# Optimization experiments

Hardware: AMD Instinct MI355X
Metric: run time of the kernel (lower is better)

The kernel has to match this reference:

```python
import jax, jax.numpy as jnp
import numpy as np

B, L, H_IN = 2, 512, 768
E = 256          # hidden_size
N = 12           # num_labels


def setup_inputs() -> dict:
    key = jax.random.key(0)
    ks = jax.random.split(key, 10)
    lim_in = 1.0 / np.sqrt(H_IN)
    lim_e = 1.0 / np.sqrt(E)
    lim_2e = 1.0 / np.sqrt(2 * E)
    return {
        "x":    jax.random.normal(ks[0], (B, L, H_IN), dtype=jnp.float32),
        "sW":   jax.random.uniform(ks[1], (E, H_IN), jnp.float32, -lim_in, lim_in),
        "sb":   jax.random.uniform(ks[2], (E,), jnp.float32, -lim_in, lim_in),
        "tW":   jax.random.uniform(ks[3], (E, H_IN), jnp.float32, -lim_in, lim_in),
        "tb":   jax.random.uniform(ks[4], (E,), jnp.float32, -lim_in, lim_in),
        "f2W":  jax.random.uniform(ks[5], (E, 2 * E), jnp.float32, -lim_2e, lim_2e),
        "f2b":  jax.random.uniform(ks[6], (E,), jnp.float32, -lim_2e, lim_2e),
        "f3W":  jax.random.normal(ks[7], (N, E), dtype=jnp.float32),  # init_weights: normal_
        "f3b":  jax.random.uniform(ks[8], (N,), jnp.float32, -lim_e, lim_e),
        "blW":  jax.random.normal(ks[9], (E * N, E), dtype=jnp.float32),  # bi_linear, no bias
    }


def reference(x, sW, sb, tW, tb, f2W, f2b, f3W, f3b, blW):
    b, l, _ = x.shape
    s = jax.nn.relu(x @ sW.T + sb)  # [B,L,E]
    t = jax.nn.relu(x @ tW.T + tb)  # [B,L,E]
    # biaffine term: key[b,s,e,n] = (s @ blW.T) reshaped, then key @ t^T
    key = (s @ blW.T).reshape(b, l, E, N)             # [B,L,E,N]
    out1 = jnp.einsum('bsen,ble->bsnl', key, t)       # [B,S,N,L]
    # pairwise concat-MLP, decomposed: cat(u,v) @ f2W.T == u@Wu.T + v@Wv.T
    Wu, Wv = f2W[:, :E], f2W[:, E:]
    su = s @ Wu.T                                     # [B,L,E]
    tv = t @ Wv.T                                     # [B,L,E]
    h = jax.nn.relu(su[:, :, None, :] + tv[:, None, :, :] + f2b)  # [B,L,L,E]
    out2 = h @ f3W.T + f3b                            # [B,L,L,N]
    out2 = jnp.transpose(out2, (0, 1, 3, 2))          # [B,L,N,L]
    return out1 + out2
```

## Files before the change

kernel.cpp:

```cpp
#include <hip/hip_runtime.h>
#include <hip/hip_bf16.h>


typedef unsigned short u16;
typedef __attribute__((ext_vector_type(8))) short    s16x8;
typedef __attribute__((ext_vector_type(8))) _Float16 f16x8;
typedef __attribute__((ext_vector_type(4))) float    f32x4;

__device__ inline u16 f2h(float f) { return __builtin_bit_cast(u16, (_Float16)f); }

__device__ inline void barrier_lds() {
    __builtin_amdgcn_sched_barrier(0);
    asm volatile("s_waitcnt lgkmcnt(0)" ::: "memory");
    __builtin_amdgcn_s_barrier();
    __builtin_amdgcn_sched_barrier(0);
}

__device__ inline s16x8 cvt2(float4 a, float4 b) {
    f16x8 h;
    h[0] = (_Float16)a.x; h[1] = (_Float16)a.y; h[2] = (_Float16)a.z; h[3] = (_Float16)a.w;
    h[4] = (_Float16)b.x; h[5] = (_Float16)b.y; h[6] = (_Float16)b.z; h[7] = (_Float16)b.w;
    return __builtin_bit_cast(s16x8, h);
}

__device__ inline f16x8 relu8(f16x8 v) {
#if __has_builtin(__builtin_elementwise_max)
    f16x8 z = {};
    return __builtin_elementwise_max(v, z);
#else
#pragma unroll
    for (int q = 0; q < 8; ++q) v[q] = v[q] > (_Float16)0.f ? v[q] : (_Float16)0.f;
    return v;
#endif
}

__device__ inline f32x4 mfma_f16(s16x8 a, s16x8 b, f32x4 c) {
    return __builtin_amdgcn_mfma_f32_16x16x32_f16(
        __builtin_bit_cast(f16x8, a), __builtin_bit_cast(f16x8, b), c, 0, 0, 0);
}
__device__ inline f32x4 mfma_f16v(f16x8 a, s16x8 b, f32x4 c) {
    return __builtin_amdgcn_mfma_f32_16x16x32_f16(a, __builtin_bit_cast(f16x8, b), c, 0, 0, 0);
}

__global__ __launch_bounds__(256, 3)
void prep_kernel(const float* __restrict__ x, const float* __restrict__ sW,
                 const float* __restrict__ tW, const float* __restrict__ sb,
                 const float* __restrict__ tb, const float* __restrict__ f2W,
                 const float* __restrict__ blW, const float* __restrict__ f3W,
                 u16* __restrict__ STb, u16* __restrict__ blkw, u16* __restrict__ f3wb)
{
    if (blockIdx.x >= 256) {
        int idx = (blockIdx.x - 256) * 256 + threadIdx.x;
        float4 v;
        u16* dst;
        if (idx < 229376) {
            int i4 = idx * 4;
            int r = i4 >> 8, k = i4 & 255;
            const float* src;
            if (r < 3072)      { int n = r >> 8, e = r & 255; src = &blW[(e * 12 + n) * 256 + k]; }
            else if (r < 3328) { src = &f2W[(r - 3072) * 512 + k]; }
            else               { src = &f2W[(r - 3328) * 512 + 256 + k]; }
            v = *(const float4*)src;
            dst = &blkw[i4];
        } else {
            int i4 = (idx - 229376) * 4;
            int row = i4 >> 8, e = i4 & 255;
            if (row < 12) v = *(const float4*)&f3W[row * 256 + e];
            else          v = make_float4(0.f, 0.f, 0.f, 0.f);
            dst = &f3wb[i4];
        }
        ushort4 o;
        o.x = f2h(v.x); o.y = f2h(v.y); o.z = f2h(v.z); o.w = f2h(v.w);
        *(ushort4*)dst = o;
        return;
    }
    __shared__ u16 As[64 * 72];
    __shared__ u16 Bs[32 * 72];
    const int tid = threadIdx.x;
    const int g = blockIdx.x;
    const int xcd = g & 7, slot = g >> 3;
    const int m0 = (((xcd << 1) | (slot >> 4))) * 64;
    const int n0 = (slot & 15) * 32;
    const int w = tid >> 6, l = tid & 63;
    const int wr = (w >> 1) * 32, wc = (w & 1) * 16;
    const int lr = l & 15, lg = l >> 4;
    const int srow = tid >> 2, kq = tid & 3;

    const float* ap = &x[(size_t)(m0 + srow) * 768 + kq * 16];
    const bool bstg = (tid < 128);
    const float* bp = nullptr;
    if (bstg) {
        int br = n0 + (tid >> 2);
        bp = (br < 256) ? &sW[(size_t)br * 768 + kq * 16]
                        : &tW[(size_t)(br - 256) * 768 + kq * 16];
    }
    float4 ra0 = *(const float4*)(ap + 0),  ra1 = *(const float4*)(ap + 4);
    float4 ra2 = *(const float4*)(ap + 8),  ra3 = *(const float4*)(ap + 12);
    float4 rb0, rb1, rb2, rb3;
    if (bstg) {
        rb0 = *(const float4*)(bp + 0);  rb1 = *(const float4*)(bp + 4);
        rb2 = *(const float4*)(bp + 8);  rb3 = *(const float4*)(bp + 12);
    }

    f32x4 acc[2] = {};
    for (int k0 = 0; k0 < 768; k0 += 64) {
        barrier_lds();
        *(s16x8*)&As[srow * 72 + kq * 16]     = cvt2(ra0, ra1);
        *(s16x8*)&As[srow * 72 + kq * 16 + 8] = cvt2(ra2, ra3);
        if (bstg) {
            *(s16x8*)&Bs[(tid >> 2) * 72 + kq * 16]     = cvt2(rb0, rb1);
            *(s16x8*)&Bs[(tid >> 2) * 72 + kq * 16 + 8] = cvt2(rb2, rb3);
        }
        barrier_lds();
        if (k0 + 64 < 768) {
            ra0 = *(const float4*)(ap + k0 + 64 + 0);  ra1 = *(const float4*)(ap + k0 + 64 + 4);
            ra2 = *(const float4*)(ap + k0 + 64 + 8);  ra3 = *(const float4*)(ap + k0 + 64 + 12);
            if (bstg) {
                rb0 = *(const float4*)(bp + k0 + 64 + 0);  rb1 = *(const float4*)(bp + k0 + 64 + 4);
                rb2 = *(const float4*)(bp + k0 + 64 + 8);  rb3 = *(const float4*)(bp + k0 + 64 + 12);
            }
        }
#pragma unroll
        for (int kk = 0; kk < 64; kk += 32) {
            s16x8 af[2], bf;
            af[0] = *(const s16x8*)&As[(wr      + lr) * 72 + kk + lg * 8];
            af[1] = *(const s16x8*)&As[(wr + 16 + lr) * 72 + kk + lg * 8];
            bf    = *(const s16x8*)&Bs[(wc      + lr) * 72 + kk + lg * 8];
            acc[0] = mfma_f16(af[0], bf, acc[0]);
            acc[1] = mfma_f16(af[1], bf, acc[1]);
        }
    }
#pragma unroll
    for (int fi = 0; fi < 2; ++fi) {
#pragma unroll
        for (int r = 0; r < 4; ++r) {
            int grow = m0 + wr + fi * 16 + lg * 4 + r;
            int gcol = n0 + wc + lr;
            float bias = (gcol < 256) ? sb[gcol] : tb[gcol - 256];
            float v = fmaxf(acc[fi][r] + bias, 0.f);
            STb[(size_t)grow * 512 + gcol] = f2h(v);
        }
    }
}

__global__ __launch_bounds__(256, 6)
void gemm_kst(const u16* __restrict__ STb, const u16* __restrict__ BLKW,
              const float* __restrict__ f2b,
              u16* __restrict__ KEYF, u16* __restrict__ SUp, u16* __restrict__ TVp)
{
    __shared__ u16 As[64 * 72];
    __shared__ u16 Bs[64 * 72];
    const int tid = threadIdx.x;
    const int lin = blockIdx.x + blockIdx.y * 56;
    const int xcd = lin & 7, slot = lin >> 3;
    const int n0 = (xcd * 7 + (slot >> 4)) * 64;
    const int m0 = (slot & 15) * 64;
    const int w = tid >> 6, l = tid & 63;
    const int wr = (w >> 1) * 32, wc = (w & 1) * 32;
    const int lr = l & 15, lg = l >> 4;
    const int srow = tid >> 2, kq = tid & 3;

    const u16* A = STb + (n0 >= 3328 ? 256 : 0);
    const u16* ap = &A[(size_t)(m0 + srow) * 512];
    const u16* bp = &BLKW[(size_t)(n0 + srow) * 256];
    s16x8 ra0 = *(const s16x8*)&ap[kq * 8];
    s16x8 ra1 = *(const s16x8*)&ap[(kq + 4) * 8];
    s16x8 rb0 = *(const s16x8*)&bp[kq * 8];
    s16x8 rb1 = *(const s16x8*)&bp[(kq + 4) * 8];

    f32x4 acc[2][2] = {};
    for (int k0 = 0; k0 < 256; k0 += 64) {
        barrier_lds();
        *(s16x8*)&As[srow * 72 + kq * 8]       = ra0;
        *(s16x8*)&As[srow * 72 + (kq + 4) * 8] = ra1;
        *(s16x8*)&Bs[srow * 72 + kq * 8]       = rb0;
        *(s16x8*)&Bs[srow * 72 + (kq + 4) * 8] = rb1;
        barrier_lds();
        if (k0 + 64 < 256) {
            ra0 = *(const s16x8*)&ap[k0 + 64 + kq * 8];
            ra1 = *(const s16x8*)&ap[k0 + 64 + (kq + 4) * 8];
            rb0 = *(const s16x8*)&bp[k0 + 64 + kq * 8];
            rb1 = *(const s16x8*)&bp[k0 + 64 + (kq + 4) * 8];
        }
#pragma unroll
        for (int kk = 0; kk < 64; kk += 32) {
            s16x8 af[2], bf[2];
            af[0] = *(const s16x8*)&As[(wr      + lr) * 72 + kk + lg * 8];
            af[1] = *(const s16x8*)&As[(wr + 16 + lr) * 72 + kk + lg * 8];
            bf[0] = *(const s16x8*)&Bs[(wc      + lr) * 72 + kk + lg * 8];
            bf[1] = *(const s16x8*)&Bs[(wc + 16 + lr) * 72 + kk + lg * 8];
#pragma unroll
            for (int fi = 0; fi < 2; ++fi)
#pragma unroll
                for (int fj = 0; fj < 2; ++fj)
                    acc[fi][fj] = mfma_f16(af[fi], bf[fj], acc[fi][fj]);
        }
    }
#pragma unroll
    for (int fi = 0; fi < 2; ++fi) {
#pragma unroll
        for (int fj = 0; fj < 2; ++fj) {
#pragma unroll
            for (int r = 0; r < 4; ++r) {
                int grow = m0 + wr + fi * 16 + lg * 4 + r;
                int gcol = n0 + wc + fj * 16 + lr;
                float v = acc[fi][fj][r];
                if (gcol < 3072) {
                    int n = gcol >> 8, e = gcol & 255;
                    int g2 = grow >> 4, li = grow & 15;
                    int it = e >> 5, sub = (e >> 3) & 3, eo = e & 7;
                    KEYF[((((size_t)n * 64 + g2) * 8 + it) * 64 + sub * 16 + li) * 8 + eo] = f2h(v);
                } else if (gcol < 3328) {
                    SUp[(size_t)grow * 256 + (gcol - 3072)] = f2h(v);
                } else {
                    TVp[(size_t)grow * 256 + (gcol - 3328)] = f2h(v + f2b[gcol - 3328]);
                }
            }
        }
    }
}

__global__ __launch_bounds__(512, 4)
void fused_out(const u16* __restrict__ KEYF, const u16* __restrict__ STb,
               const u16* __restrict__ SUp, const u16* __restrict__ TVp,
               const u16* __restrict__ F3WH, const float* __restrict__ f3b,
               float* __restrict__ out)
{
    __shared__ __align__(16) char smem[26624];
    u16* lds = (u16*)smem;
    const int TC0 = 0, SUC0 = 5120, F3C = 6400;

    const int tid = threadIdx.x;
    const int w = tid >> 6, l = tid & 63;

    const int lin  = blockIdx.x + (blockIdx.y << 3) + (blockIdx.z << 8);
    const int orig = (lin & 7) * 64 + (lin >> 3);
    const int j0 = (orig & 7) * 64;
    const int i0 = ((orig >> 3) & 31) * 16;
    const int b  = orig >> 8;

    const int lr = l & 15, lg = l >> 4;
    const int wn = w & 3, jh = w >> 2;

    const u16* src1 = nullptr; int d1 = 0, dstride = 0;
    if (tid < 256) {
        int jj = tid >> 2, qq = tid & 3;
        src1 = STb + (size_t)(b * 512 + j0 + jj) * 512 + 256 + qq * 8;
        d1 = TC0 + jj * 40 + qq * 8;
        dstride = 2560;
    } else if (tid < 320) {
        int q = tid - 256, ii = q >> 2, qq = q & 3;
        src1 = SUp + (size_t)(b * 512 + i0 + ii) * 256 + qq * 8;
        d1 = SUC0 + ii * 40 + qq * 8;
        dstride = 640;
    }
    const bool stg = (tid < 320);

    {
        int row = tid >> 5, qq = tid & 31;
        *(s16x8*)&lds[F3C + row * 264 + qq * 8] = *(const s16x8*)&F3WH[row * 256 + qq * 8];
    }

    const int gblk = b * 32 + (i0 >> 4);
    const u16* kfb0 = KEYF + ((size_t)((3 * wn + 0) * 64 + gblk) * 8) * 512 + l * 8;
    const u16* kfb1 = KEYF + ((size_t)((3 * wn + 1) * 64 + gblk) * 8) * 512 + l * 8;
    const u16* kfb2 = KEYF + ((size_t)((3 * wn + 2) * 64 + gblk) * 8) * 512 + l * 8;
    const u16* tvb = TVp + (size_t)(b * 512 + j0 + w * 8) * 256 + lg * 8;

    s16x8 r1 = {};
    if (stg) {
        r1 = *(const s16x8*)src1;
        *(s16x8*)&lds[d1] = r1;
        r1 = *(const s16x8*)(src1 + 32);
    }
    s16x8 kf0 = *(const s16x8*)kfb0;
    s16x8 kf1 = *(const s16x8*)kfb1;
    s16x8 kf2 = *(const s16x8*)kfb2;
    barrier_lds();

    f32x4 acc1[3][2] = {};
    f32x4 acc2[8]    = {};

#pragma unroll
    for (int it = 0; it < 8; ++it) {
        const int cur = it & 1, nxt = cur ^ 1;
        if (it < 7 && stg) *(s16x8*)&lds[d1 + nxt * dstride] = r1;
        s16x8 tf0 = *(const s16x8*)&lds[TC0 + cur * 2560 + (jh * 32      + lr) * 40 + lg * 8];
        s16x8 tf1 = *(const s16x8*)&lds[TC0 + cur * 2560 + (jh * 32 + 16 + lr) * 40 + lg * 8];
        acc1[0][0] = mfma_f16(kf0, tf0, acc1[0][0]);
        acc1[0][1] = mfma_f16(kf0, tf1, acc1[0][1]);
        acc1[1][0] = mfma_f16(kf1, tf0, acc1[1][0]);
        acc1[1][1] = mfma_f16(kf1, tf1, acc1[1][1]);
        acc1[2][0] = mfma_f16(kf2, tf0, acc1[2][0]);
        acc1[2][1] = mfma_f16(kf2, tf1, acc1[2][1]);
        if (it < 7) {
            kf0 = *(const s16x8*)(kfb0 + (it + 1) * 512);
            kf1 = *(const s16x8*)(kfb1 + (it + 1) * 512);
            kf2 = *(const s16x8*)(kfb2 + (it + 1) * 512);
        }
        f16x8 sv = __builtin_bit_cast(f16x8,
            *(const s16x8*)&lds[SUC0 + cur * 640 + lr * 40 + lg * 8]);
        s16x8 f3fr = *(const s16x8*)&lds[F3C + lr * 264 + it * 32 + lg * 8];
#pragma unroll
        for (int jj = 0; jj < 8; ++jj) {
            f16x8 tv8 = __builtin_bit_cast(f16x8,
                *(const s16x8*)(tvb + jj * 256 + it * 32));
            f16x8 hv = relu8(sv + tv8);
            acc2[jj] = mfma_f16v(hv, f3fr, acc2[jj]);
        }
        if (it < 6 && stg) r1 = *(const s16x8*)(src1 + (it + 2) * 32);
        barrier_lds();
    }

    float* mg = (float*)smem;
#pragma unroll
    for (int nc = 0; nc < 2; ++nc) {
        __syncthreads();
        const int nb = nc * 6;
        const int lrp = lr - nb;
        if (lrp >= 0 && lrp < 6) {
#pragma unroll
            for (int r = 0; r < 4; ++r) {
                int i = lg * 4 + r;
                f32x4 v0, v1;
                v0[0] = acc2[0][r]; v0[1] = acc2[1][r]; v0[2] = acc2[2][r]; v0[3] = acc2[3][r];
                v1[0] = acc2[4][r]; v1[1] = acc2[5][r]; v1[2] = acc2[6][r]; v1[3] = acc2[7][r];
                *(f32x4*)&mg[lrp * 1092 + i * 68 + w * 8]     = v0;
                *(f32x4*)&mg[lrp * 1092 + i * 68 + w * 8 + 4] = v1;
            }
        }
        __syncthreads();
        if ((wn >> 1) == nc) {
#pragma unroll
            for (int a = 0; a < 3; ++a) {
                int n = 3 * wn + a;
                float fb = f3b[n];
#pragma unroll
                for (int fj = 0; fj < 2; ++fj) {
                    int j = jh * 32 + fj * 16 + lr;
#pragma unroll
                    for (int r = 0; r < 4; ++r) {
                        int i = lg * 4 + r;
                        float vv = acc1[a][fj][r] + mg[(n - nb) * 1092 + i * 68 + j] + fb;
                        out[(((size_t)(b * 512 + i0 + i)) * 12 + n) * 512 + j0 + j] = vv;
                    }
                }
            }
        }
    }
}

extern "C" void kernel_launch(void* const* d_in, const int* in_sizes, int n_in,
                              void* d_out, int out_size, void* d_ws, size_t ws_size,
                              hipStream_t stream)
{
    const float* x   = (const float*)d_in[0];
    const float* sW  = (const float*)d_in[1];
    const float* sb  = (const float*)d_in[2];
    const float* tW  = (const float*)d_in[3];
    const float* tb  = (const float*)d_in[4];
    const float* f2W = (const float*)d_in[5];
    const float* f2b = (const float*)d_in[6];
    const float* f3W = (const float*)d_in[7];
    const float* f3b = (const float*)d_in[8];
    const float* blW = (const float*)d_in[9];
    float* out = (float*)d_out;

    char* p = (char*)d_ws;
    u16* STb   = (u16*)p; p += 1048576;
    u16* blkw  = (u16*)p; p += 1835008;
    u16* KEYF  = (u16*)p; p += 6291456;
    u16* SUp   = (u16*)p; p += 524288;
    u16* TVp   = (u16*)p; p += 524288;
    u16* f3wbg = (u16*)p; p += 8192;

    prep_kernel<<<1156, 256, 0, stream>>>(x, sW, tW, sb, tb, f2W, blW, f3W,
                                          STb, blkw, f3wbg);
    gemm_kst<<<dim3(56, 16), 256, 0, stream>>>(STb, blkw, f2b, KEYF, SUp, TVp);
    fused_out<<<dim3(8, 32, 2), 512, 0, stream>>>(KEYF, STb, SUp, TVp, f3wbg, f3b, out);
}
```

Baseline: 50.46 us.

## Halve fused_out tile width to 32 columns with 4 waves and prefetch TV

The fused output kernel now uses 16x32 output tiles with 256 threads (4 waves) instead of 16x64 with 512 threads, so the grid doubles. Each wave now owns three labels across all 32 columns. The TV loads are prefetched into registers one iteration ahead instead of being read inline. The epilogue merges all 12 labels in one LDS pass instead of two. The aim is more blocks for load balance, shorter global load latency and fewer barriers, at the cost of reloading KEYF and SU per smaller tile and higher register pressure.

```diff
diff --git a/kernel.cpp b/kernel.cpp
--- a/kernel.cpp
+++ b/kernel.cpp
@@ -220,51 +220,54 @@
     }
 }
 
-__global__ __launch_bounds__(512, 4)
+__global__ __launch_bounds__(256, 3)
 void fused_out(const u16* __restrict__ KEYF, const u16* __restrict__ STb,
                const u16* __restrict__ SUp, const u16* __restrict__ TVp,
                const u16* __restrict__ F3WH, const float* __restrict__ f3b,
                float* __restrict__ out)
 {
-    __shared__ __align__(16) char smem[26624];
+    __shared__ __align__(16) char smem[27904];
     u16* lds = (u16*)smem;
-    const int TC0 = 0, SUC0 = 5120, F3C = 6400;
+    const int TC0 = 0, SUC0 = 2560, F3C = 3840;
 
     const int tid = threadIdx.x;
     const int w = tid >> 6, l = tid & 63;
 
-    const int lin  = blockIdx.x + (blockIdx.y << 3) + (blockIdx.z << 8);
-    const int orig = (lin & 7) * 64 + (lin >> 3);
-    const int j0 = (orig & 7) * 64;
-    const int i0 = ((orig >> 3) & 31) * 16;
-    const int b  = orig >> 8;
+    const int lin  = blockIdx.x + (blockIdx.y << 4) + (blockIdx.z << 9);
+    const int orig = (lin & 7) * 128 + (lin >> 3);
+    const int j0 = (orig & 15) * 32;
+    const int i0 = ((orig >> 4) & 31) * 16;
+    const int b  = orig >> 9;
 
     const int lr = l & 15, lg = l >> 4;
-    const int wn = w & 3, jh = w >> 2;
 
     const u16* src1 = nullptr; int d1 = 0, dstride = 0;
-    if (tid < 256) {
+    if (tid < 128) {
         int jj = tid >> 2, qq = tid & 3;
         src1 = STb + (size_t)(b * 512 + j0 + jj) * 512 + 256 + qq * 8;
         d1 = TC0 + jj * 40 + qq * 8;
-        dstride = 2560;
-    } else if (tid < 320) {
-        int q = tid - 256, ii = q >> 2, qq = q & 3;
+        dstride = 1280;
+    } else if (tid < 192) {
+        int q = tid - 128, ii = q >> 2, qq = q & 3;
         src1 = SUp + (size_t)(b * 512 + i0 + ii) * 256 + qq * 8;
         d1 = SUC0 + ii * 40 + qq * 8;
         dstride = 640;
     }
-    const bool stg = (tid < 320);
+    const bool stg = (tid < 192);
 
     {
-        int row = tid >> 5, qq = tid & 31;
-        *(s16x8*)&lds[F3C + row * 264 + qq * 8] = *(const s16x8*)&F3WH[row * 256 + qq * 8];
+#pragma unroll
+        for (int rr = 0; rr < 2; ++rr) {
+            int g = tid + 256 * rr;
+            int row = g >> 5, qq = g & 31;
+            *(s16x8*)&lds[F3C + row * 264 + qq * 8] = *(const s16x8*)&F3WH[row * 256 + qq * 8];
+        }
     }
 
     const int gblk = b * 32 + (i0 >> 4);
-    const u16* kfb0 = KEYF + ((size_t)((3 * wn + 0) * 64 + gblk) * 8) * 512 + l * 8;
-    const u16* kfb1 = KEYF + ((size_t)((3 * wn + 1) * 64 + gblk) * 8) * 512 + l * 8;
-    const u16* kfb2 = KEYF + ((size_t)((3 * wn + 2) * 64 + gblk) * 8) * 512 + l * 8;
+    const u16* kfb0 = KEYF + ((size_t)((3 * w + 0) * 64 + gblk) * 8) * 512 + l * 8;
+    const u16* kfb1 = KEYF + ((size_t)((3 * w + 1) * 64 + gblk) * 8) * 512 + l * 8;
+    const u16* kfb2 = KEYF + ((size_t)((3 * w + 2) * 64 + gblk) * 8) * 512 + l * 8;
     const u16* tvb = TVp + (size_t)(b * 512 + j0 + w * 8) * 256 + lg * 8;
 
     s16x8 r1 = {};
@@ -276,6 +279,9 @@
     s16x8 kf0 = *(const s16x8*)kfb0;
     s16x8 kf1 = *(const s16x8*)kfb1;
     s16x8 kf2 = *(const s16x8*)kfb2;
+    s16x8 tv[8];
+#pragma unroll
+    for (int jj = 0; jj < 8; ++jj) tv[jj] = *(const s16x8*)(tvb + jj * 256);
     barrier_lds();
 
     f32x4 acc1[3][2] = {};
@@ -285,8 +291,8 @@
     for (int it = 0; it < 8; ++it) {
         const int cur = it & 1, nxt = cur ^ 1;
         if (it < 7 && stg) *(s16x8*)&lds[d1 + nxt * dstride] = r1;
-        s16x8 tf0 = *(const s16x8*)&lds[TC0 + cur * 2560 + (jh * 32      + lr) * 40 + lg * 8];
-        s16x8 tf1 = *(const s16x8*)&lds[TC0 + cur * 2560 + (jh * 32 + 16 + lr) * 40 + lg * 8];
+        s16x8 tf0 = *(const s16x8*)&lds[TC0 + cur * 1280 + lr * 40 + lg * 8];
+        s16x8 tf1 = *(const s16x8*)&lds[TC0 + cur * 1280 + (16 + lr) * 40 + lg * 8];
         acc1[0][0] = mfma_f16(kf0, tf0, acc1[0][0]);
         acc1[0][1] = mfma_f16(kf0, tf1, acc1[0][1]);
         acc1[1][0] = mfma_f16(kf1, tf0, acc1[1][0]);
@@ -303,48 +309,43 @@
         s16x8 f3fr = *(const s16x8*)&lds[F3C + lr * 264 + it * 32 + lg * 8];
 #pragma unroll
         for (int jj = 0; jj < 8; ++jj) {
-            f16x8 tv8 = __builtin_bit_cast(f16x8,
-                *(const s16x8*)(tvb + jj * 256 + it * 32));
-            f16x8 hv = relu8(sv + tv8);
+            f16x8 hv = relu8(sv + __builtin_bit_cast(f16x8, tv[jj]));
             acc2[jj] = mfma_f16v(hv, f3fr, acc2[jj]);
         }
+        if (it < 7) {
+#pragma unroll
+            for (int jj = 0; jj < 8; ++jj)
+                tv[jj] = *(const s16x8*)(tvb + jj * 256 + (it + 1) * 32);
+        }
         if (it < 6 && stg) r1 = *(const s16x8*)(src1 + (it + 2) * 32);
         barrier_lds();
     }
 
     float* mg = (float*)smem;
-#pragma unroll
-    for (int nc = 0; nc < 2; ++nc) {
-        __syncthreads();
-        const int nb = nc * 6;
-        const int lrp = lr - nb;
-        if (lrp >= 0 && lrp < 6) {
+    if (lr < 12) {
+#pragma unroll
+        for (int r = 0; r < 4; ++r) {
+            int i = lg * 4 + r;
+            f32x4 v0, v1;
+            v0[0] = acc2[0][r]; v0[1] = acc2[1][r]; v0[2] = acc2[2][r]; v0[3] = acc2[3][r];
+            v1[0] = acc2[4][r]; v1[1] = acc2[5][r]; v1[2] = acc2[6][r]; v1[3] = acc2[7][r];
+            *(f32x4*)&mg[lr * 580 + i * 36 + w * 8]     = v0;
+            *(f32x4*)&mg[lr * 580 + i * 36 + w * 8 + 4] = v1;
+        }
+    }
+    __syncthreads();
+#pragma unroll
+    for (int a = 0; a < 3; ++a) {
+        int n = 3 * w + a;
+        float fb = f3b[n];
+#pragma unroll
+        for (int fj = 0; fj < 2; ++fj) {
+            int j = fj * 16 + lr;
 #pragma unroll
             for (int r = 0; r < 4; ++r) {
                 int i = lg * 4 + r;
-                f32x4 v0, v1;
-                v0[0] = acc2[0][r]; v0[1] = acc2[1][r]; v0[2] = acc2[2][r]; v0[3] = acc2[3][r];
-                v1[0] = acc2[4][r]; v1[1] = acc2[5][r]; v1[2] = acc2[6][r]; v1[3] = acc2[7][r];
-                *(f32x4*)&mg[lrp * 1092 + i * 68 + w * 8]     = v0;
-                *(f32x4*)&mg[lrp * 1092 + i * 68 + w * 8 + 4] = v1;
-            }
-        }
-        __syncthreads();
-        if ((wn >> 1) == nc) {
-#pragma unroll
-            for (int a = 0; a < 3; ++a) {
-                int n = 3 * wn + a;
-                float fb = f3b[n];
-#pragma unroll
-                for (int fj = 0; fj < 2; ++fj) {
-                    int j = jh * 32 + fj * 16 + lr;
-#pragma unroll
-                    for (int r = 0; r < 4; ++r) {
-                        int i = lg * 4 + r;
-                        float vv = acc1[a][fj][r] + mg[(n - nb) * 1092 + i * 68 + j] + fb;
-                        out[(((size_t)(b * 512 + i0 + i)) * 12 + n) * 512 + j0 + j] = vv;
-                    }
-                }
+                float vv = acc1[a][fj][r] + mg[n * 580 + i * 36 + j] + fb;
+                out[(((size_t)(b * 512 + i0 + i)) * 12 + n) * 512 + j0 + j] = vv;
             }
         }
     }
@@ -377,5 +378,5 @@
     prep_kernel<<<1156, 256, 0, stream>>>(x, sW, tW, sb, tb, f2W, blW, f3W,
                                           STb, blkw, f3wbg);
     gemm_kst<<<dim3(56, 16), 256, 0, stream>>>(STb, blkw, f2b, KEYF, SUp, TVp);
-    fused_out<<<dim3(8, 32, 2), 512, 0, stream>>>(KEYF, STb, SUp, TVp, f3wbg, f3b, out);
-}
+    fused_out<<<dim3(16, 32, 2), 256, 0, stream>>>(KEYF, STb, SUp, TVp, f3wbg, f3b, out);
+}
```

Result: faster. 46.40 us (-8.1%).
